# Optimization experiments

Hardware: AMD Instinct MI355X
Metric: run time of the kernel (lower is better)

## Reference

```python
import jax, jax.numpy as jnp
import numpy as np

N_NODES = 100000
N_EDGES = 1600000
HID = 128
EPS = 1e-5

def _bn(x, gamma, beta):
    # BatchNorm1d in training mode: biased batch stats over node dim
    mu = jnp.mean(x, axis=0)
    var = jnp.mean((x - mu) ** 2, axis=0)
    return (x - mu) * jax.lax.rsqrt(var + EPS) * gamma + beta

def _gcn(x, src, dst, norm, n, W, b):
    # PyG GCNConv: h = x @ W, symmetric-normalized aggregation with self-loops, + bias
    h = x @ W
    msg = h[src] * norm[:, None]            # [E+N, H] gather + scale
    out = jax.ops.segment_sum(msg, dst, num_segments=n)
    return out + b

def _gcn_norm(edge_index, n):
    # append self-loops, compute D^{-1/2}[src] * D^{-1/2}[dst]
    loop = jnp.arange(n, dtype=edge_index.dtype)
    src = jnp.concatenate([edge_index[0], loop])
    dst = jnp.concatenate([edge_index[1], loop])
    deg = jax.ops.segment_sum(jnp.ones_like(dst, dtype=jnp.float32), dst, num_segments=n)
    dinv = jax.lax.rsqrt(jnp.maximum(deg, 1.0))  # deg >= 1 due to self loops
    norm = dinv[src] * dinv[dst]
    return src, dst, norm

def setup_inputs() -> dict:
    key = jax.random.key(0)
    ks = jax.random.split(key, 20)
    def lin(k, fan_in, fan_out):
        bound = 1.0 / np.sqrt(fan_in)
        kw, kb = jax.random.split(k)
        W = jax.random.uniform(kw, (fan_in, fan_out), jnp.float32, -bound, bound)
        b = jax.random.uniform(kb, (fan_out,), jnp.float32, -bound, bound)
        return W, b
    x = jax.random.normal(ks[0], (N_NODES, 2), jnp.float32)
    edge_index = jax.random.randint(ks[1], (2, N_EDGES), 0, N_NODES, jnp.int32)
    We, be = lin(ks[2], 2, HID)
    W1, b1 = lin(ks[3], HID, HID)
    W2, b2 = lin(ks[4], HID, HID)
    W3, b3 = lin(ks[5], HID, HID)
    Wf1, bf1 = lin(ks[6], HID, 32)
    Wf2, bf2 = lin(ks[7], 32, 2)
    ones = lambda n: jnp.ones((n,), jnp.float32)
    zeros = lambda n: jnp.zeros((n,), jnp.float32)
    return dict(x=x, edge_index=edge_index, We=We, be=be,
                W1=W1, b1=b1, g1=ones(HID), bt1=zeros(HID),
                W2=W2, b2=b2, g2=ones(HID), bt2=zeros(HID),
                W3=W3, b3=b3, g3=ones(HID), bt3=zeros(HID),
                Wf1=Wf1, bf1=bf1, gf=ones(32), btf=zeros(32),
                Wf2=Wf2, bf2=bf2)

def reference(x, edge_index, We, be, W1, b1, g1, bt1, W2, b2, g2, bt2,
              W3, b3, g3, bt3, Wf1, bf1, gf, btf, Wf2, bf2):
    n = x.shape[0]
    src, dst, norm = _gcn_norm(edge_index, n)
    h = jax.nn.relu(x @ We + be)
    # block 1 with residual
    h1 = jax.nn.relu(_bn(_gcn(h, src, dst, norm, n, W1, b1), g1, bt1)) + h
    # block 2
    h2 = jax.nn.relu(_bn(_gcn(h1, src, dst, norm, n, W2, b2), g2, bt2)) + h1
    # block 3
    h3 = jax.nn.relu(_bn(_gcn(h2, src, dst, norm, n, W3, b3), g3, bt3)) + h2
    f = jax.nn.relu(_bn(h3 @ Wf1 + bf1, gf, btf))
    # dropout is identity in eval mode
    return jnp.tanh(f @ Wf2 + bf2)
```

## Files before the change

kernel.cpp:

```cpp
#include <hip/hip_runtime.h>
#include <hip/hip_fp16.h>
#include <math.h>

#define HID 128
#define EPS 1e-5f
#define BK 64
#define MAXNBK 2048
#define NSTRIPE 16
#define PADK 136

typedef _Float16 half8 __attribute__((ext_vector_type(8)));
typedef float f32x4 __attribute__((ext_vector_type(4)));


__global__ __launch_bounds__(256) void k_bhist(const int* __restrict__ dst, int* __restrict__ bcount,
                                               int e, int nbk) {
    __shared__ int hist[MAXNBK];
    for (int i = threadIdx.x; i < nbk; i += 256) hist[i] = 0;
    __syncthreads();
    int base = blockIdx.x * 4096;
    int end = min(base + 4096, e);
    for (int i = base + threadIdx.x; i < end; i += 256) atomicAdd(&hist[dst[i] >> 6], 1);
    __syncthreads();
    for (int i = threadIdx.x; i < nbk; i += 256) {
        int c = hist[i];
        if (c) atomicAdd(&bcount[i * 16], c);
    }
}

__global__ __launch_bounds__(1024) void k_bscan(const int* __restrict__ bcount, int* __restrict__ boffs,
                                                int* __restrict__ bcur, int nbk, int e) {
    __shared__ int lds[1024];
    int tid = threadIdx.x;
    int i0 = 2 * tid, i1 = 2 * tid + 1;
    int a = (i0 < nbk) ? bcount[i0 * 16] : 0;
    int b = (i1 < nbk) ? bcount[i1 * 16] : 0;
    lds[tid] = a + b;
    __syncthreads();
    for (int off = 1; off < 1024; off <<= 1) {
        int v = (tid >= off) ? lds[tid - off] : 0;
        __syncthreads();
        lds[tid] += v;
        __syncthreads();
    }
    int excl = lds[tid] - (a + b);
    if (i0 < nbk) { boffs[i0] = excl;     bcur[i0 * 16] = excl; }
    if (i1 < nbk) { boffs[i1] = excl + a; bcur[i1 * 16] = excl + a; }
    if (tid == 1023) boffs[nbk] = e;
}

__global__ __launch_bounds__(1024) void k_bscatter(const int* __restrict__ src, const int* __restrict__ dst,
                                                   int* __restrict__ bcur, int* __restrict__ btmp,
                                                   int e, int nbk) {
    __shared__ int hist[MAXNBK];
    int tid = threadIdx.x;
    for (int i = tid; i < nbk; i += 1024) hist[i] = 0;
    __syncthreads();
    int per = (e + gridDim.x - 1) / gridDim.x;
    int base = blockIdx.x * per;
    int end = min(base + per, e);
    for (int i = base + tid; i < end; i += 1024) atomicAdd(&hist[dst[i] >> 6], 1);
    __syncthreads();
    for (int i = tid; i < nbk; i += 1024) {
        int c = hist[i];
        hist[i] = c ? atomicAdd(&bcur[i * 16], c) : 0;
    }
    __syncthreads();
    for (int i = base + tid; i < end; i += 1024) {
        int d = dst[i];
        int pos = atomicAdd(&hist[d >> 6], 1);
        btmp[pos] = (src[i] << 6) | (d & 63);
    }
}

__global__ __launch_bounds__(256) void k_bsort(const int* __restrict__ btmp, const int* __restrict__ boffs,
                                               int* __restrict__ csr, int* __restrict__ offs,
                                               float* __restrict__ dinv, int n, int etot) {
    __shared__ int cnt[BK];
    __shared__ int cur[BK];
    int b = blockIdx.x, tid = threadIdx.x;
    if (tid < BK) cnt[tid] = 0;
    __syncthreads();
    int e0 = boffs[b], e1 = boffs[b + 1];
    for (int i = e0 + tid; i < e1; i += 256) atomicAdd(&cnt[btmp[i] & 63], 1);
    __syncthreads();
    if (tid == 0) {
        int run = 0;
        for (int d = 0; d < BK; ++d) { cur[d] = run; run += cnt[d]; }
    }
    __syncthreads();
    if (tid < BK) {
        int node = b * BK + tid;
        if (node < n) {
            offs[node] = e0 + cur[tid];
            dinv[node] = rsqrtf((float)(cnt[tid] + 1));
        }
    }
    if (b == 0 && tid == 0) offs[n] = etot;
    __syncthreads();
    for (int i = e0 + tid; i < e1; i += 256) {
        int p = btmp[i];
        int pos = e0 + atomicAdd(&cur[p & 63], 1);
        csr[pos] = p >> 6;
    }
}


__global__ void k_prepw(const float* __restrict__ W, _Float16* __restrict__ Wt) {
    int idx = blockIdx.x * 256 + threadIdx.x;
    int k = idx >> 7, nn = idx & 127;
    Wt[nn * 128 + k] = (_Float16)W[k * 128 + nn];
}

__global__ void k_prepwf(const float* __restrict__ W, _Float16* __restrict__ Wt) {
    int idx = blockIdx.x * 256 + threadIdx.x;
    int k = idx >> 5, nn = idx & 31;
    Wt[nn * 128 + k] = (_Float16)W[k * 32 + nn];
}


__global__ void k_embed(const float* __restrict__ x, const float* __restrict__ We,
                        const float* __restrict__ be, float* __restrict__ h, int n) {
    int i = blockIdx.x * 256 + threadIdx.x;
    if (i >= n * HID) return;
    int node = i >> 7, j = i & 127;
    float v = x[2 * node] * We[j] + x[2 * node + 1] * We[HID + j] + be[j];
    h[i] = fmaxf(v, 0.f);
}


__global__ __launch_bounds__(256) void k_mm1(const float* __restrict__ h, const _Float16* __restrict__ Wt,
                                             const float* __restrict__ dinv, __half2* __restrict__ th, int n) {
    __shared__ __attribute__((aligned(16))) _Float16 Ah[64][PADK];
    __shared__ __attribute__((aligned(16))) _Float16 Bh[128][PADK];
    int tid = threadIdx.x;
    int nb = blockIdx.x * 64;
    const float4* h4 = (const float4*)h;
#pragma unroll
    for (int r = 0; r < 8; ++r) {
        int idx = r * 256 + tid;
        int ni = idx >> 5, k4 = idx & 31;
        int node = nb + ni;
        float4 v = make_float4(0.f, 0.f, 0.f, 0.f);
        if (node < n) v = h4[(size_t)node * 32 + k4];
        union { __half2 h2[2]; uint2 u; } pk;
        pk.h2[0] = __floats2half2_rn(v.x, v.y);
        pk.h2[1] = __floats2half2_rn(v.z, v.w);
        *(uint2*)&Ah[ni][k4 * 4] = pk.u;
    }
    const uint4* wt4 = (const uint4*)Wt;
#pragma unroll
    for (int r = 0; r < 8; ++r) {
        int idx = r * 256 + tid;
        int row = idx >> 4, ch = idx & 15;
        *(uint4*)&Bh[row][ch * 8] = wt4[row * 16 + ch];
    }
    __syncthreads();
    int lane = tid & 63, w = tid >> 6;
    int mrow = lane & 15, quad = lane >> 4;
    f32x4 acc[8];
#pragma unroll
    for (int t = 0; t < 8; ++t) acc[t] = (f32x4){0.f, 0.f, 0.f, 0.f};
#pragma unroll
    for (int kc = 0; kc < 4; ++kc) {
        half8 av = *(half8*)&Ah[w * 16 + mrow][kc * 32 + quad * 8];
#pragma unroll
        for (int t = 0; t < 8; ++t) {
            half8 bv = *(half8*)&Bh[t * 16 + mrow][kc * 32 + quad * 8];
            acc[t] = __builtin_amdgcn_mfma_f32_16x16x32_f16(av, bv, acc[t], 0, 0, 0);
        }
    }
    float dv[4];
#pragma unroll
    for (int r = 0; r < 4; ++r) {
        int node = nb + w * 16 + quad * 4 + r;
        dv[r] = (node < n) ? dinv[node] : 0.f;
    }
    __syncthreads();
#pragma unroll
    for (int t = 0; t < 8; ++t)
#pragma unroll
        for (int r = 0; r < 4; ++r)
            Ah[w * 16 + quad * 4 + r][t * 16 + mrow] = (_Float16)(acc[t][r] * dv[r]);
    __syncthreads();
#pragma unroll
    for (int it = 0; it < 4; ++it) {
        int idx = it * 256 + tid;
        int row = idx >> 4, ch = idx & 15;
        int node = nb + row;
        if (node < n)
            ((uint4*)th)[(size_t)node * 16 + ch] = *(uint4*)&Ah[row][ch * 8];
    }
}


__global__ __launch_bounds__(256) void k_mmf(const float* __restrict__ agg, float* __restrict__ h,
                                             const float* __restrict__ A, const float* __restrict__ Cc,
                                             const _Float16* __restrict__ Wt, const float* __restrict__ dinv,
                                             __half2* __restrict__ th, int n) {
    __shared__ __attribute__((aligned(16))) _Float16 Ah[64][PADK];
    __shared__ __attribute__((aligned(16))) _Float16 Bh[128][PADK];
    __shared__ float As[128], Cs[128];
    int tid = threadIdx.x;
    int nb = blockIdx.x * 64;
    if (tid < 128) { As[tid] = A[tid]; Cs[tid] = Cc[tid]; }
    __syncthreads();
    const float4* a4p = (const float4*)agg;
    float4* h4 = (float4*)h;
#pragma unroll
    for (int r = 0; r < 8; ++r) {
        int idx = r * 256 + tid;
        int ni = idx >> 5, k4 = idx & 31;
        int node = nb + ni;
        float4 v = make_float4(0.f, 0.f, 0.f, 0.f);
        if (node < n) {
            float4 a = a4p[(size_t)node * 32 + k4];
            float4 ho = h4[(size_t)node * 32 + k4];
            float4 aa = *((const float4*)&As[k4 * 4]);
            float4 cc = *((const float4*)&Cs[k4 * 4]);
            v.x = fmaxf(a.x * aa.x + cc.x, 0.f) + ho.x;
            v.y = fmaxf(a.y * aa.y + cc.y, 0.f) + ho.y;
            v.z = fmaxf(a.z * aa.z + cc.z, 0.f) + ho.z;
            v.w = fmaxf(a.w * aa.w + cc.w, 0.f) + ho.w;
            h4[(size_t)node * 32 + k4] = v;
        }
        union { __half2 h2[2]; uint2 u; } pk;
        pk.h2[0] = __floats2half2_rn(v.x, v.y);
        pk.h2[1] = __floats2half2_rn(v.z, v.w);
        *(uint2*)&Ah[ni][k4 * 4] = pk.u;
    }
    const uint4* wt4 = (const uint4*)Wt;
#pragma unroll
    for (int r = 0; r < 8; ++r) {
        int idx = r * 256 + tid;
        int row = idx >> 4, ch = idx & 15;
        *(uint4*)&Bh[row][ch * 8] = wt4[row * 16 + ch];
    }
    __syncthreads();
    int lane = tid & 63, w = tid >> 6;
    int mrow = lane & 15, quad = lane >> 4;
    f32x4 acc[8];
#pragma unroll
    for (int t = 0; t < 8; ++t) acc[t] = (f32x4){0.f, 0.f, 0.f, 0.f};
#pragma unroll
    for (int kc = 0; kc < 4; ++kc) {
        half8 av = *(half8*)&Ah[w * 16 + mrow][kc * 32 + quad * 8];
#pragma unroll
        for (int t = 0; t < 8; ++t) {
            half8 bv = *(half8*)&Bh[t * 16 + mrow][kc * 32 + quad * 8];
            acc[t] = __builtin_amdgcn_mfma_f32_16x16x32_f16(av, bv, acc[t], 0, 0, 0);
        }
    }
    float dv[4];
#pragma unroll
    for (int r = 0; r < 4; ++r) {
        int node = nb + w * 16 + quad * 4 + r;
        dv[r] = (node < n) ? dinv[node] : 0.f;
    }
    __syncthreads();
#pragma unroll
    for (int t = 0; t < 8; ++t)
#pragma unroll
        for (int r = 0; r < 4; ++r)
            Ah[w * 16 + quad * 4 + r][t * 16 + mrow] = (_Float16)(acc[t][r] * dv[r]);
    __syncthreads();
#pragma unroll
    for (int it = 0; it < 4; ++it) {
        int idx = it * 256 + tid;
        int row = idx >> 4, ch = idx & 15;
        int node = nb + row;
        if (node < n)
            ((uint4*)th)[(size_t)node * 16 + ch] = *(uint4*)&Ah[row][ch * 8];
    }
}


__global__ __launch_bounds__(256) void k_mmh(const float* __restrict__ agg, const float* __restrict__ h,
                                             const float* __restrict__ A, const float* __restrict__ Cc,
                                             const _Float16* __restrict__ Wt, const float* __restrict__ bias,
                                             float* __restrict__ tf,
                                             float* __restrict__ S, float* __restrict__ SS, int n) {
    __shared__ __attribute__((aligned(16))) _Float16 Ah[64][PADK];
    __shared__ __attribute__((aligned(16))) _Float16 Bh[32][PADK];
    __shared__ float Ds[64][36];
    __shared__ float As[128], Cs[128];
    __shared__ float sredS[4][8][4], sredQ[4][8][4];
    int tid = threadIdx.x;
    int nb = blockIdx.x * 64;
    if (tid < 128) { As[tid] = A[tid]; Cs[tid] = Cc[tid]; }
    __syncthreads();
    const float4* a4p = (const float4*)agg;
    const float4* h4 = (const float4*)h;
#pragma unroll
    for (int r = 0; r < 8; ++r) {
        int idx = r * 256 + tid;
        int ni = idx >> 5, k4 = idx & 31;
        int node = nb + ni;
        float4 v = make_float4(0.f, 0.f, 0.f, 0.f);
        if (node < n) {
            float4 a = a4p[(size_t)node * 32 + k4];
            float4 ho = h4[(size_t)node * 32 + k4];
            float4 aa = *((const float4*)&As[k4 * 4]);
            float4 cc = *((const float4*)&Cs[k4 * 4]);
            v.x = fmaxf(a.x * aa.x + cc.x, 0.f) + ho.x;
            v.y = fmaxf(a.y * aa.y + cc.y, 0.f) + ho.y;
            v.z = fmaxf(a.z * aa.z + cc.z, 0.f) + ho.z;
            v.w = fmaxf(a.w * aa.w + cc.w, 0.f) + ho.w;
        }
        union { __half2 h2[2]; uint2 u; } pk;
        pk.h2[0] = __floats2half2_rn(v.x, v.y);
        pk.h2[1] = __floats2half2_rn(v.z, v.w);
        *(uint2*)&Ah[ni][k4 * 4] = pk.u;
    }
    const uint4* wt4 = (const uint4*)Wt;
#pragma unroll
    for (int r = 0; r < 2; ++r) {
        int idx = r * 256 + tid;
        int row = idx >> 4, ch = idx & 15;
        *(uint4*)&Bh[row][ch * 8] = wt4[row * 16 + ch];
    }
    __syncthreads();
    int lane = tid & 63, w = tid >> 6;
    int mrow = lane & 15, quad = lane >> 4;
    f32x4 acc[2];
    acc[0] = (f32x4){0.f, 0.f, 0.f, 0.f};
    acc[1] = (f32x4){0.f, 0.f, 0.f, 0.f};
#pragma unroll
    for (int kc = 0; kc < 4; ++kc) {
        half8 av = *(half8*)&Ah[w * 16 + mrow][kc * 32 + quad * 8];
#pragma unroll
        for (int t = 0; t < 2; ++t) {
            half8 bv = *(half8*)&Bh[t * 16 + mrow][kc * 32 + quad * 8];
            acc[t] = __builtin_amdgcn_mfma_f32_16x16x32_f16(av, bv, acc[t], 0, 0, 0);
        }
    }
#pragma unroll
    for (int t = 0; t < 2; ++t)
#pragma unroll
        for (int r = 0; r < 4; ++r)
            Ds[w * 16 + quad * 4 + r][t * 16 + mrow] = acc[t][r];
    __syncthreads();
    float ps0 = 0.f, ps1 = 0.f, ps2 = 0.f, ps3 = 0.f;
    float pq0 = 0.f, pq1 = 0.f, pq2 = 0.f, pq3 = 0.f;
    int c4 = tid & 7;
    float4 bb = ((const float4*)bias)[c4];
#pragma unroll
    for (int it = 0; it < 2; ++it) {
        int idx = it * 256 + tid;
        int row = idx >> 3;
        int node = nb + row;
        if (node < n) {
            float v0 = Ds[row][c4 * 4 + 0] + bb.x;
            float v1 = Ds[row][c4 * 4 + 1] + bb.y;
            float v2 = Ds[row][c4 * 4 + 2] + bb.z;
            float v3 = Ds[row][c4 * 4 + 3] + bb.w;
            *((float4*)&tf[(size_t)node * 32 + c4 * 4]) = make_float4(v0, v1, v2, v3);
            ps0 += v0; ps1 += v1; ps2 += v2; ps3 += v3;
            pq0 += v0 * v0; pq1 += v1 * v1; pq2 += v2 * v2; pq3 += v3 * v3;
        }
    }
#pragma unroll
    for (int off = 8; off < 64; off <<= 1) {
        ps0 += __shfl_down(ps0, off); ps1 += __shfl_down(ps1, off);
        ps2 += __shfl_down(ps2, off); ps3 += __shfl_down(ps3, off);
        pq0 += __shfl_down(pq0, off); pq1 += __shfl_down(pq1, off);
        pq2 += __shfl_down(pq2, off); pq3 += __shfl_down(pq3, off);
    }
    if (lane < 8) {
        sredS[w][lane][0] = ps0; sredS[w][lane][1] = ps1; sredS[w][lane][2] = ps2; sredS[w][lane][3] = ps3;
        sredQ[w][lane][0] = pq0; sredQ[w][lane][1] = pq1; sredQ[w][lane][2] = pq2; sredQ[w][lane][3] = pq3;
    }
    __syncthreads();
    if (tid < 32) {
        int cc4 = tid >> 2, j = tid & 3;
        float s = sredS[0][cc4][j] + sredS[1][cc4][j] + sredS[2][cc4][j] + sredS[3][cc4][j];
        float q = sredQ[0][cc4][j] + sredQ[1][cc4][j] + sredQ[2][cc4][j] + sredQ[3][cc4][j];
        int stripe = (blockIdx.x & (NSTRIPE - 1)) * 128;
        atomicAdd(&S[stripe + tid], s);
        atomicAdd(&SS[stripe + tid], q);
    }
}


__global__ __launch_bounds__(256) void k_agg(const __half2* __restrict__ t, const int* __restrict__ offs,
                                             const int* __restrict__ csr, const float* __restrict__ dinv,
                                             const float* __restrict__ bias, float* __restrict__ out,
                                             float* __restrict__ S, float* __restrict__ SS, int n) {
    __shared__ float ls[4][128];
    __shared__ float lss[4][128];
    int tid = threadIdx.x;
    int lane = tid & 63, w = tid >> 6;
    int sub = lane >> 5, fl = lane & 31;
    const uint2* t4 = (const uint2*)t;
    float4 bb = ((const float4*)bias)[fl];
    float s0 = 0.f, s1 = 0.f, s2 = 0.f, s3 = 0.f;
    float q0 = 0.f, q1 = 0.f, q2 = 0.f, q3 = 0.f;
    float selfm = (sub == 0) ? 1.f : 0.f;
    int ngrp = (n + 3) >> 2;
    for (int grp = blockIdx.x; grp < ngrp; grp += gridDim.x) {
        int node = grp * 4 + w;
        if (node < n) {
            uint2 rv = t4[(size_t)node * 32 + fl];
            float2 f0 = __half22float2(*(__half2*)&rv.x);
            float2 f1 = __half22float2(*(__half2*)&rv.y);
            float a0 = f0.x * selfm, a1 = f0.y * selfm, a2 = f1.x * selfm, a3 = f1.y * selfm;
            int e0 = offs[node], e1 = offs[node + 1];
            for (int e = e0; e < e1; e += 8) {
                int i0 = e + sub, i1 = e + 2 + sub, i2 = e + 4 + sub, i3 = e + 6 + sub;
                int c0 = csr[min(i0, e1 - 1)];
                int c1 = csr[min(i1, e1 - 1)];
                int c2 = csr[min(i2, e1 - 1)];
                int c3 = csr[min(i3, e1 - 1)];
                uint2 r0 = t4[(size_t)c0 * 32 + fl];
                uint2 r1 = t4[(size_t)c1 * 32 + fl];
                uint2 r2 = t4[(size_t)c2 * 32 + fl];
                uint2 r3 = t4[(size_t)c3 * 32 + fl];
                float m0 = (i0 < e1) ? 1.f : 0.f;
                float m1 = (i1 < e1) ? 1.f : 0.f;
                float m2 = (i2 < e1) ? 1.f : 0.f;
                float m3 = (i3 < e1) ? 1.f : 0.f;
                float2 g0 = __half22float2(*(__half2*)&r0.x), g1 = __half22float2(*(__half2*)&r0.y);
                a0 += m0 * g0.x; a1 += m0 * g0.y; a2 += m0 * g1.x; a3 += m0 * g1.y;
                g0 = __half22float2(*(__half2*)&r1.x); g1 = __half22float2(*(__half2*)&r1.y);
                a0 += m1 * g0.x; a1 += m1 * g0.y; a2 += m1 * g1.x; a3 += m1 * g1.y;
                g0 = __half22float2(*(__half2*)&r2.x); g1 = __half22float2(*(__half2*)&r2.y);
                a0 += m2 * g0.x; a1 += m2 * g0.y; a2 += m2 * g1.x; a3 += m2 * g1.y;
                g0 = __half22float2(*(__half2*)&r3.x); g1 = __half22float2(*(__half2*)&r3.y);
                a0 += m3 * g0.x; a1 += m3 * g0.y; a2 += m3 * g1.x; a3 += m3 * g1.y;
            }
            a0 += __shfl_down(a0, 32);
            a1 += __shfl_down(a1, 32);
            a2 += __shfl_down(a2, 32);
            a3 += __shfl_down(a3, 32);
            if (sub == 0) {
                float di = dinv[node];
                float v0 = a0 * di + bb.x, v1 = a1 * di + bb.y;
                float v2 = a2 * di + bb.z, v3 = a3 * di + bb.w;
                ((float4*)out)[(size_t)node * 32 + fl] = make_float4(v0, v1, v2, v3);
                s0 += v0; s1 += v1; s2 += v2; s3 += v3;
                q0 += v0 * v0; q1 += v1 * v1; q2 += v2 * v2; q3 += v3 * v3;
            }
        }
    }
    if (sub == 0) {
        ((float4*)&ls[w][0])[fl] = make_float4(s0, s1, s2, s3);
        ((float4*)&lss[w][0])[fl] = make_float4(q0, q1, q2, q3);
    }
    __syncthreads();
    if (tid < 128) {
        float s = ls[0][tid] + ls[1][tid] + ls[2][tid] + ls[3][tid];
        float q = lss[0][tid] + lss[1][tid] + lss[2][tid] + lss[3][tid];
        int stripe = (blockIdx.x & (NSTRIPE - 1)) * 128;
        atomicAdd(&S[stripe + tid], s);
        atomicAdd(&SS[stripe + tid], q);
    }
}


__global__ void k_bn_finalize(const float* __restrict__ S, const float* __restrict__ SS,
                              const float* __restrict__ g, const float* __restrict__ bt,
                              float* __restrict__ A, float* __restrict__ C, int n, int hid, int nstripe) {
    int j = threadIdx.x;
    if (j >= hid) return;
    float s = 0.f, q = 0.f;
    for (int k = 0; k < nstripe; ++k) { s += S[k * 128 + j]; q += SS[k * 128 + j]; }
    float mu = s / (float)n;
    float var = q / (float)n - mu * mu;
    float inv = rsqrtf(var + EPS);
    A[j] = g[j] * inv;
    C[j] = bt[j] - mu * g[j] * inv;
}


__global__ void k_final(const float* __restrict__ tf, const float* __restrict__ A,
                        const float* __restrict__ C, const float* __restrict__ Wf2,
                        const float* __restrict__ bf2, float* __restrict__ out, int n) {
    int node = blockIdx.x * 256 + threadIdx.x;
    if (node >= n) return;
    float o0 = bf2[0], o1 = bf2[1];
    const float4* t4 = (const float4*)(tf + (size_t)node * 32);
#pragma unroll
    for (int q = 0; q < 8; ++q) {
        float4 v = t4[q];
        float vv[4] = {v.x, v.y, v.z, v.w};
#pragma unroll
        for (int r = 0; r < 4; ++r) {
            int j = q * 4 + r;
            float f = fmaxf(vv[r] * A[j] + C[j], 0.f);
            o0 += f * Wf2[2 * j];
            o1 += f * Wf2[2 * j + 1];
        }
    }
    out[2 * node] = tanhf(o0);
    out[2 * node + 1] = tanhf(o1);
}


extern "C" void kernel_launch(void* const* d_in, const int* in_sizes, int n_in,
                              void* d_out, int out_size, void* d_ws, size_t ws_size,
                              hipStream_t stream) {
    const float* x   = (const float*)d_in[0];
    const int*   ei  = (const int*)d_in[1];
    const float* We  = (const float*)d_in[2];
    const float* be  = (const float*)d_in[3];
    const float* W1  = (const float*)d_in[4];
    const float* b1  = (const float*)d_in[5];
    const float* g1  = (const float*)d_in[6];
    const float* bt1 = (const float*)d_in[7];
    const float* W2  = (const float*)d_in[8];
    const float* b2  = (const float*)d_in[9];
    const float* g2  = (const float*)d_in[10];
    const float* bt2 = (const float*)d_in[11];
    const float* W3  = (const float*)d_in[12];
    const float* b3  = (const float*)d_in[13];
    const float* g3  = (const float*)d_in[14];
    const float* bt3 = (const float*)d_in[15];
    const float* Wf1 = (const float*)d_in[16];
    const float* bf1 = (const float*)d_in[17];
    const float* gf  = (const float*)d_in[18];
    const float* btf = (const float*)d_in[19];
    const float* Wf2 = (const float*)d_in[20];
    const float* bf2 = (const float*)d_in[21];
    float* out = (float*)d_out;

    const int n = in_sizes[0] / 2;
    const int e = in_sizes[1] / 2;
    const int* srcp = ei;
    const int* dstp = ei + e;
    const int nbk = (n + BK - 1) / BK;

    char* p = (char*)d_ws;
    auto alloc = [&](size_t bytes) { void* r = (void*)p; p += (bytes + 255) & ~(size_t)255; return r; };
    int*       bcount = (int*)alloc((size_t)nbk * 16 * 4);
    int*       boffs  = (int*)alloc((size_t)(nbk + 1) * 4);
    int*       bcur   = (int*)alloc((size_t)nbk * 16 * 4);
    int*       btmp   = (int*)alloc((size_t)e * 4);
    int*       csr    = (int*)alloc((size_t)e * 4);
    int*       offs   = (int*)alloc((size_t)(n + 1) * 4);
    float*     dinv   = (float*)alloc((size_t)n * 4);
    float*     h      = (float*)alloc((size_t)n * HID * 4);
    __half2*   th     = (__half2*)alloc((size_t)n * HID * 2);
    float*     agg    = (float*)alloc((size_t)n * HID * 4);
    float*     tf     = (float*)alloc((size_t)n * 32 * 4);
    float*     bnS    = (float*)alloc(NSTRIPE * 128 * 4);
    float*     bnSS   = (float*)alloc(NSTRIPE * 128 * 4);
    float*     bnA    = (float*)alloc(HID * 4);
    float*     bnC    = (float*)alloc(HID * 4);
    _Float16*  wt1    = (_Float16*)alloc(128 * 128 * 2);
    _Float16*  wt2    = (_Float16*)alloc(128 * 128 * 2);
    _Float16*  wt3    = (_Float16*)alloc(128 * 128 * 2);
    _Float16*  wtf    = (_Float16*)alloc(32 * 128 * 2);

    hipMemsetAsync(bcount, 0, (size_t)nbk * 16 * 4, stream);
    k_bhist<<<(e + 4095) / 4096, 256, 0, stream>>>(dstp, bcount, e, nbk);
    k_bscan<<<1, 1024, 0, stream>>>(bcount, boffs, bcur, nbk, e);
    k_bscatter<<<256, 1024, 0, stream>>>(srcp, dstp, bcur, btmp, e, nbk);
    k_bsort<<<nbk, 256, 0, stream>>>(btmp, boffs, csr, offs, dinv, n, e);
    k_prepw<<<64, 256, 0, stream>>>(W1, wt1);
    k_prepw<<<64, 256, 0, stream>>>(W2, wt2);
    k_prepw<<<64, 256, 0, stream>>>(W3, wt3);
    k_prepwf<<<16, 256, 0, stream>>>(Wf1, wtf);
    k_embed<<<(n * HID + 255) / 256, 256, 0, stream>>>(x, We, be, h, n);

    k_mm1<<<(n + 63) / 64, 256, 0, stream>>>(h, wt1, dinv, th, n);
    hipMemsetAsync(bnS, 0, NSTRIPE * 128 * 4, stream);
    hipMemsetAsync(bnSS, 0, NSTRIPE * 128 * 4, stream);
    k_agg<<<4096, 256, 0, stream>>>(th, offs, csr, dinv, b1, agg, bnS, bnSS, n);
    k_bn_finalize<<<1, 128, 0, stream>>>(bnS, bnSS, g1, bt1, bnA, bnC, n, 128, NSTRIPE);

    k_mmf<<<(n + 63) / 64, 256, 0, stream>>>(agg, h, bnA, bnC, wt2, dinv, th, n);
    hipMemsetAsync(bnS, 0, NSTRIPE * 128 * 4, stream);
    hipMemsetAsync(bnSS, 0, NSTRIPE * 128 * 4, stream);
    k_agg<<<4096, 256, 0, stream>>>(th, offs, csr, dinv, b2, agg, bnS, bnSS, n);
    k_bn_finalize<<<1, 128, 0, stream>>>(bnS, bnSS, g2, bt2, bnA, bnC, n, 128, NSTRIPE);

    k_mmf<<<(n + 63) / 64, 256, 0, stream>>>(agg, h, bnA, bnC, wt3, dinv, th, n);
    hipMemsetAsync(bnS, 0, NSTRIPE * 128 * 4, stream);
    hipMemsetAsync(bnSS, 0, NSTRIPE * 128 * 4, stream);
    k_agg<<<4096, 256, 0, stream>>>(th, offs, csr, dinv, b3, agg, bnS, bnSS, n);
    k_bn_finalize<<<1, 128, 0, stream>>>(bnS, bnSS, g3, bt3, bnA, bnC, n, 128, NSTRIPE);

    hipMemsetAsync(bnS, 0, NSTRIPE * 128 * 4, stream);
    hipMemsetAsync(bnSS, 0, NSTRIPE * 128 * 4, stream);
    k_mmh<<<(n + 63) / 64, 256, 0, stream>>>(agg, h, bnA, bnC, wtf, bf1, tf, bnS, bnSS, n);
    k_bn_finalize<<<1, 32, 0, stream>>>(bnS, bnSS, gf, btf, bnA, bnC, n, 32, NSTRIPE);
    k_final<<<(n + 255) / 256, 256, 0, stream>>>(tf, bnA, bnC, Wf2, bf2, out, n);
}
```

Baseline: 566.0 us.

## Fuse embed into first matmul, inline BN finalize, widen aggregation gathers

The embedding kernel is folded into k_mm1, which computes relu(x@We+be) on the fly, writes h and packs it to fp16 for the MFMA. This removes one full pass writing and re-reading h. The separate BN-finalize kernels and the per-layer memsets are removed: each consumer kernel reduces the stripe sums itself, and all stats buffers are cleared by one memset. The aggregation kernel now uses 16-byte gathers with 16 lanes per row and 4 edge sub-groups, which means more shuffle reduction and more registers per thread.

```diff
diff --git a/kernel.cpp b/kernel.cpp
--- a/kernel.cpp
+++ b/kernel.cpp
@@ -119,30 +119,36 @@
 }
 
 
-__global__ void k_embed(const float* __restrict__ x, const float* __restrict__ We,
-                        const float* __restrict__ be, float* __restrict__ h, int n) {
-    int i = blockIdx.x * 256 + threadIdx.x;
-    if (i >= n * HID) return;
-    int node = i >> 7, j = i & 127;
-    float v = x[2 * node] * We[j] + x[2 * node + 1] * We[HID + j] + be[j];
-    h[i] = fmaxf(v, 0.f);
-}
-
-
-__global__ __launch_bounds__(256) void k_mm1(const float* __restrict__ h, const _Float16* __restrict__ Wt,
-                                             const float* __restrict__ dinv, __half2* __restrict__ th, int n) {
+__global__ __launch_bounds__(256) void k_mm1(const float* __restrict__ x, const float* __restrict__ We,
+                                             const float* __restrict__ be, const _Float16* __restrict__ Wt,
+                                             const float* __restrict__ dinv, __half2* __restrict__ th,
+                                             float* __restrict__ h, int n) {
     __shared__ __attribute__((aligned(16))) _Float16 Ah[64][PADK];
     __shared__ __attribute__((aligned(16))) _Float16 Bh[128][PADK];
+    __shared__ float W0s[128], W1s[128], bes[128];
     int tid = threadIdx.x;
     int nb = blockIdx.x * 64;
-    const float4* h4 = (const float4*)h;
+    if (tid < 128) { W0s[tid] = We[tid]; W1s[tid] = We[128 + tid]; bes[tid] = be[tid]; }
+    __syncthreads();
+    float4* h4 = (float4*)h;
+    const float2* x2 = (const float2*)x;
 #pragma unroll
     for (int r = 0; r < 8; ++r) {
         int idx = r * 256 + tid;
         int ni = idx >> 5, k4 = idx & 31;
         int node = nb + ni;
         float4 v = make_float4(0.f, 0.f, 0.f, 0.f);
-        if (node < n) v = h4[(size_t)node * 32 + k4];
+        if (node < n) {
+            float2 xx = x2[node];
+            float4 w0 = *((const float4*)&W0s[k4 * 4]);
+            float4 w1 = *((const float4*)&W1s[k4 * 4]);
+            float4 bb = *((const float4*)&bes[k4 * 4]);
+            v.x = fmaxf(xx.x * w0.x + xx.y * w1.x + bb.x, 0.f);
+            v.y = fmaxf(xx.x * w0.y + xx.y * w1.y + bb.y, 0.f);
+            v.z = fmaxf(xx.x * w0.z + xx.y * w1.z + bb.z, 0.f);
+            v.w = fmaxf(xx.x * w0.w + xx.y * w1.w + bb.w, 0.f);
+            h4[(size_t)node * 32 + k4] = v;
+        }
         union { __half2 h2[2]; uint2 u; } pk;
         pk.h2[0] = __floats2half2_rn(v.x, v.y);
         pk.h2[1] = __floats2half2_rn(v.z, v.w);
@@ -195,7 +201,8 @@
 
 
 __global__ __launch_bounds__(256) void k_mmf(const float* __restrict__ agg, float* __restrict__ h,
-                                             const float* __restrict__ A, const float* __restrict__ Cc,
+                                             const float* __restrict__ S, const float* __restrict__ SS,
+                                             const float* __restrict__ g, const float* __restrict__ bt,
                                              const _Float16* __restrict__ Wt, const float* __restrict__ dinv,
                                              __half2* __restrict__ th, int n) {
     __shared__ __attribute__((aligned(16))) _Float16 Ah[64][PADK];
@@ -203,7 +210,16 @@
     __shared__ float As[128], Cs[128];
     int tid = threadIdx.x;
     int nb = blockIdx.x * 64;
-    if (tid < 128) { As[tid] = A[tid]; Cs[tid] = Cc[tid]; }
+    if (tid < 128) {
+        float s = 0.f, q = 0.f;
+#pragma unroll
+        for (int k = 0; k < NSTRIPE; ++k) { s += S[k * 128 + tid]; q += SS[k * 128 + tid]; }
+        float mu = s / (float)n;
+        float var = q / (float)n - mu * mu;
+        float inv = rsqrtf(var + EPS);
+        As[tid] = g[tid] * inv;
+        Cs[tid] = bt[tid] - mu * g[tid] * inv;
+    }
     __syncthreads();
     const float4* a4p = (const float4*)agg;
     float4* h4 = (float4*)h;
@@ -276,7 +292,8 @@
 
 
 __global__ __launch_bounds__(256) void k_mmh(const float* __restrict__ agg, const float* __restrict__ h,
-                                             const float* __restrict__ A, const float* __restrict__ Cc,
+                                             const float* __restrict__ Sin, const float* __restrict__ SSin,
+                                             const float* __restrict__ g, const float* __restrict__ bt,
                                              const _Float16* __restrict__ Wt, const float* __restrict__ bias,
                                              float* __restrict__ tf,
                                              float* __restrict__ S, float* __restrict__ SS, int n) {
@@ -287,7 +304,16 @@
     __shared__ float sredS[4][8][4], sredQ[4][8][4];
     int tid = threadIdx.x;
     int nb = blockIdx.x * 64;
-    if (tid < 128) { As[tid] = A[tid]; Cs[tid] = Cc[tid]; }
+    if (tid < 128) {
+        float s = 0.f, q = 0.f;
+#pragma unroll
+        for (int k = 0; k < NSTRIPE; ++k) { s += Sin[k * 128 + tid]; q += SSin[k * 128 + tid]; }
+        float mu = s / (float)n;
+        float var = q / (float)n - mu * mu;
+        float inv = rsqrtf(var + EPS);
+        As[tid] = g[tid] * inv;
+        Cs[tid] = bt[tid] - mu * g[tid] * inv;
+    }
     __syncthreads();
     const float4* a4p = (const float4*)agg;
     const float4* h4 = (const float4*)h;
@@ -390,61 +416,85 @@
     __shared__ float lss[4][128];
     int tid = threadIdx.x;
     int lane = tid & 63, w = tid >> 6;
-    int sub = lane >> 5, fl = lane & 31;
-    const uint2* t4 = (const uint2*)t;
-    float4 bb = ((const float4*)bias)[fl];
-    float s0 = 0.f, s1 = 0.f, s2 = 0.f, s3 = 0.f;
-    float q0 = 0.f, q1 = 0.f, q2 = 0.f, q3 = 0.f;
+    int sub = lane >> 4, fl = lane & 15;
+    const uint4* t8 = (const uint4*)t;
+    float4 bb0 = ((const float4*)bias)[fl * 2];
+    float4 bb1 = ((const float4*)bias)[fl * 2 + 1];
+    float st[8] = {0.f, 0.f, 0.f, 0.f, 0.f, 0.f, 0.f, 0.f};
+    float qt[8] = {0.f, 0.f, 0.f, 0.f, 0.f, 0.f, 0.f, 0.f};
     float selfm = (sub == 0) ? 1.f : 0.f;
     int ngrp = (n + 3) >> 2;
     for (int grp = blockIdx.x; grp < ngrp; grp += gridDim.x) {
         int node = grp * 4 + w;
         if (node < n) {
-            uint2 rv = t4[(size_t)node * 32 + fl];
-            float2 f0 = __half22float2(*(__half2*)&rv.x);
-            float2 f1 = __half22float2(*(__half2*)&rv.y);
-            float a0 = f0.x * selfm, a1 = f0.y * selfm, a2 = f1.x * selfm, a3 = f1.y * selfm;
+            float a[8];
+            {
+                uint4 rv = t8[(size_t)node * 16 + fl];
+                float2 f0 = __half22float2(*(__half2*)&rv.x);
+                float2 f1 = __half22float2(*(__half2*)&rv.y);
+                float2 f2 = __half22float2(*(__half2*)&rv.z);
+                float2 f3 = __half22float2(*(__half2*)&rv.w);
+                a[0] = f0.x * selfm; a[1] = f0.y * selfm; a[2] = f1.x * selfm; a[3] = f1.y * selfm;
+                a[4] = f2.x * selfm; a[5] = f2.y * selfm; a[6] = f3.x * selfm; a[7] = f3.y * selfm;
+            }
             int e0 = offs[node], e1 = offs[node + 1];
-            for (int e = e0; e < e1; e += 8) {
-                int i0 = e + sub, i1 = e + 2 + sub, i2 = e + 4 + sub, i3 = e + 6 + sub;
+            for (int e = e0; e < e1; e += 16) {
+                int i0 = e + sub, i1 = e + 4 + sub, i2 = e + 8 + sub, i3 = e + 12 + sub;
                 int c0 = csr[min(i0, e1 - 1)];
                 int c1 = csr[min(i1, e1 - 1)];
                 int c2 = csr[min(i2, e1 - 1)];
                 int c3 = csr[min(i3, e1 - 1)];
-                uint2 r0 = t4[(size_t)c0 * 32 + fl];
-                uint2 r1 = t4[(size_t)c1 * 32 + fl];
-                uint2 r2 = t4[(size_t)c2 * 32 + fl];
-                uint2 r3 = t4[(size_t)c3 * 32 + fl];
+                uint4 r0 = t8[(size_t)c0 * 16 + fl];
+                uint4 r1 = t8[(size_t)c1 * 16 + fl];
+                uint4 r2 = t8[(size_t)c2 * 16 + fl];
+                uint4 r3 = t8[(size_t)c3 * 16 + fl];
                 float m0 = (i0 < e1) ? 1.f : 0.f;
                 float m1 = (i1 < e1) ? 1.f : 0.f;
                 float m2 = (i2 < e1) ? 1.f : 0.f;
                 float m3 = (i3 < e1) ? 1.f : 0.f;
-                float2 g0 = __half22float2(*(__half2*)&r0.x), g1 = __half22float2(*(__half2*)&r0.y);
-                a0 += m0 * g0.x; a1 += m0 * g0.y; a2 += m0 * g1.x; a3 += m0 * g1.y;
+                float2 g0, g1, g2, g3;
+                g0 = __half22float2(*(__half2*)&r0.x); g1 = __half22float2(*(__half2*)&r0.y);
+                g2 = __half22float2(*(__half2*)&r0.z); g3 = __half22float2(*(__half2*)&r0.w);
+                a[0] += m0 * g0.x; a[1] += m0 * g0.y; a[2] += m0 * g1.x; a[3] += m0 * g1.y;
+                a[4] += m0 * g2.x; a[5] += m0 * g2.y; a[6] += m0 * g3.x; a[7] += m0 * g3.y;
                 g0 = __half22float2(*(__half2*)&r1.x); g1 = __half22float2(*(__half2*)&r1.y);
-                a0 += m1 * g0.x; a1 += m1 * g0.y; a2 += m1 * g1.x; a3 += m1 * g1.y;
+                g2 = __half22float2(*(__half2*)&r1.z); g3 = __half22float2(*(__half2*)&r1.w);
+                a[0] += m1 * g0.x; a[1] += m1 * g0.y; a[2] += m1 * g1.x; a[3] += m1 * g1.y;
+                a[4] += m1 * g2.x; a[5] += m1 * g2.y; a[6] += m1 * g3.x; a[7] += m1 * g3.y;
                 g0 = __half22float2(*(__half2*)&r2.x); g1 = __half22float2(*(__half2*)&r2.y);
-                a0 += m2 * g0.x; a1 += m2 * g0.y; a2 += m2 * g1.x; a3 += m2 * g1.y;
+                g2 = __half22float2(*(__half2*)&r2.z); g3 = __half22float2(*(__half2*)&r2.w);
+                a[0] += m2 * g0.x; a[1] += m2 * g0.y; a[2] += m2 * g1.x; a[3] += m2 * g1.y;
+                a[4] += m2 * g2.x; a[5] += m2 * g2.y; a[6] += m2 * g3.x; a[7] += m2 * g3.y;
                 g0 = __half22float2(*(__half2*)&r3.x); g1 = __half22float2(*(__half2*)&r3.y);
-                a0 += m3 * g0.x; a1 += m3 * g0.y; a2 += m3 * g1.x; a3 += m3 * g1.y;
+                g2 = __half22float2(*(__half2*)&r3.z); g3 = __half22float2(*(__half2*)&r3.w);
+                a[0] += m3 * g0.x; a[1] += m3 * g0.y; a[2] += m3 * g1.x; a[3] += m3 * g1.y;
+                a[4] += m3 * g2.x; a[5] += m3 * g2.y; a[6] += m3 * g3.x; a[7] += m3 * g3.y;
             }
-            a0 += __shfl_down(a0, 32);
-            a1 += __shfl_down(a1, 32);
-            a2 += __shfl_down(a2, 32);
-            a3 += __shfl_down(a3, 32);
+#pragma unroll
+            for (int j = 0; j < 8; ++j) {
+                a[j] += __shfl_down(a[j], 16);
+                a[j] += __shfl_down(a[j], 32);
+            }
             if (sub == 0) {
                 float di = dinv[node];
-                float v0 = a0 * di + bb.x, v1 = a1 * di + bb.y;
-                float v2 = a2 * di + bb.z, v3 = a3 * di + bb.w;
-                ((float4*)out)[(size_t)node * 32 + fl] = make_float4(v0, v1, v2, v3);
-                s0 += v0; s1 += v1; s2 += v2; s3 += v3;
-                q0 += v0 * v0; q1 += v1 * v1; q2 += v2 * v2; q3 += v3 * v3;
+                float v0 = a[0] * di + bb0.x, v1 = a[1] * di + bb0.y;
+                float v2 = a[2] * di + bb0.z, v3 = a[3] * di + bb0.w;
+                float v4 = a[4] * di + bb1.x, v5 = a[5] * di + bb1.y;
+                float v6 = a[6] * di + bb1.z, v7 = a[7] * di + bb1.w;
+                ((float4*)out)[(size_t)node * 32 + fl * 2] = make_float4(v0, v1, v2, v3);
+                ((float4*)out)[(size_t)node * 32 + fl * 2 + 1] = make_float4(v4, v5, v6, v7);
+                st[0] += v0; st[1] += v1; st[2] += v2; st[3] += v3;
+                st[4] += v4; st[5] += v5; st[6] += v6; st[7] += v7;
+                qt[0] += v0 * v0; qt[1] += v1 * v1; qt[2] += v2 * v2; qt[3] += v3 * v3;
+                qt[4] += v4 * v4; qt[5] += v5 * v5; qt[6] += v6 * v6; qt[7] += v7 * v7;
             }
         }
     }
     if (sub == 0) {
-        ((float4*)&ls[w][0])[fl] = make_float4(s0, s1, s2, s3);
-        ((float4*)&lss[w][0])[fl] = make_float4(q0, q1, q2, q3);
+        *(float4*)&ls[w][fl * 8] = make_float4(st[0], st[1], st[2], st[3]);
+        *(float4*)&ls[w][fl * 8 + 4] = make_float4(st[4], st[5], st[6], st[7]);
+        *(float4*)&lss[w][fl * 8] = make_float4(qt[0], qt[1], qt[2], qt[3]);
+        *(float4*)&lss[w][fl * 8 + 4] = make_float4(qt[4], qt[5], qt[6], qt[7]);
     }
     __syncthreads();
     if (tid < 128) {
@@ -457,25 +507,25 @@
 }
 
 
-__global__ void k_bn_finalize(const float* __restrict__ S, const float* __restrict__ SS,
-                              const float* __restrict__ g, const float* __restrict__ bt,
-                              float* __restrict__ A, float* __restrict__ C, int n, int hid, int nstripe) {
-    int j = threadIdx.x;
-    if (j >= hid) return;
-    float s = 0.f, q = 0.f;
-    for (int k = 0; k < nstripe; ++k) { s += S[k * 128 + j]; q += SS[k * 128 + j]; }
-    float mu = s / (float)n;
-    float var = q / (float)n - mu * mu;
-    float inv = rsqrtf(var + EPS);
-    A[j] = g[j] * inv;
-    C[j] = bt[j] - mu * g[j] * inv;
-}
-
-
-__global__ void k_final(const float* __restrict__ tf, const float* __restrict__ A,
-                        const float* __restrict__ C, const float* __restrict__ Wf2,
-                        const float* __restrict__ bf2, float* __restrict__ out, int n) {
-    int node = blockIdx.x * 256 + threadIdx.x;
+__global__ __launch_bounds__(256) void k_final(const float* __restrict__ tf,
+                                               const float* __restrict__ S, const float* __restrict__ SS,
+                                               const float* __restrict__ gf, const float* __restrict__ btf,
+                                               const float* __restrict__ Wf2, const float* __restrict__ bf2,
+                                               float* __restrict__ out, int n) {
+    __shared__ float Af[32], Cf[32];
+    int tid = threadIdx.x;
+    if (tid < 32) {
+        float s = 0.f, q = 0.f;
+#pragma unroll
+        for (int k = 0; k < NSTRIPE; ++k) { s += S[k * 128 + tid]; q += SS[k * 128 + tid]; }
+        float mu = s / (float)n;
+        float var = q / (float)n - mu * mu;
+        float inv = rsqrtf(var + EPS);
+        Af[tid] = gf[tid] * inv;
+        Cf[tid] = btf[tid] - mu * gf[tid] * inv;
+    }
+    __syncthreads();
+    int node = blockIdx.x * 256 + tid;
     if (node >= n) return;
     float o0 = bf2[0], o1 = bf2[1];
     const float4* t4 = (const float4*)(tf + (size_t)node * 32);
@@ -486,7 +536,7 @@
 #pragma unroll
         for (int r = 0; r < 4; ++r) {
             int j = q * 4 + r;
-            float f = fmaxf(vv[r] * A[j] + C[j], 0.f);
+            float f = fmaxf(vv[r] * Af[j] + Cf[j], 0.f);
             o0 += f * Wf2[2 * j];
             o1 += f * Wf2[2 * j + 1];
         }
@@ -542,16 +592,19 @@
     __half2*   th     = (__half2*)alloc((size_t)n * HID * 2);
     float*     agg    = (float*)alloc((size_t)n * HID * 4);
     float*     tf     = (float*)alloc((size_t)n * 32 * 4);
-    float*     bnS    = (float*)alloc(NSTRIPE * 128 * 4);
-    float*     bnSS   = (float*)alloc(NSTRIPE * 128 * 4);
-    float*     bnA    = (float*)alloc(HID * 4);
-    float*     bnC    = (float*)alloc(HID * 4);
+    float*     bnAll  = (float*)alloc(8 * NSTRIPE * 128 * 4);
     _Float16*  wt1    = (_Float16*)alloc(128 * 128 * 2);
     _Float16*  wt2    = (_Float16*)alloc(128 * 128 * 2);
     _Float16*  wt3    = (_Float16*)alloc(128 * 128 * 2);
     _Float16*  wtf    = (_Float16*)alloc(32 * 128 * 2);
 
+    float* S0 = bnAll;             float* SS0 = bnAll + 4 * NSTRIPE * 128;
+    float* S1 = S0 + NSTRIPE*128;  float* SS1 = SS0 + NSTRIPE*128;
+    float* S2 = S1 + NSTRIPE*128;  float* SS2 = SS1 + NSTRIPE*128;
+    float* SH = S2 + NSTRIPE*128;  float* SSH = SS2 + NSTRIPE*128;
+
     hipMemsetAsync(bcount, 0, (size_t)nbk * 16 * 4, stream);
+    hipMemsetAsync(bnAll, 0, 8 * NSTRIPE * 128 * 4, stream);
     k_bhist<<<(e + 4095) / 4096, 256, 0, stream>>>(dstp, bcount, e, nbk);
     k_bscan<<<1, 1024, 0, stream>>>(bcount, boffs, bcur, nbk, e);
     k_bscatter<<<256, 1024, 0, stream>>>(srcp, dstp, bcur, btmp, e, nbk);
@@ -560,29 +613,17 @@
     k_prepw<<<64, 256, 0, stream>>>(W2, wt2);
     k_prepw<<<64, 256, 0, stream>>>(W3, wt3);
     k_prepwf<<<16, 256, 0, stream>>>(Wf1, wtf);
-    k_embed<<<(n * HID + 255) / 256, 256, 0, stream>>>(x, We, be, h, n);
-
-    k_mm1<<<(n + 63) / 64, 256, 0, stream>>>(h, wt1, dinv, th, n);
-    hipMemsetAsync(bnS, 0, NSTRIPE * 128 * 4, stream);
-    hipMemsetAsync(bnSS, 0, NSTRIPE * 128 * 4, stream);
-    k_agg<<<4096, 256, 0, stream>>>(th, offs, csr, dinv, b1, agg, bnS, bnSS, n);
-    k_bn_finalize<<<1, 128, 0, stream>>>(bnS, bnSS, g1, bt1, bnA, bnC, n, 128, NSTRIPE);
-
-    k_mmf<<<(n + 63) / 64, 256, 0, stream>>>(agg, h, bnA, bnC, wt2, dinv, th, n);
-    hipMemsetAsync(bnS, 0, NSTRIPE * 128 * 4, stream);
-    hipMemsetAsync(bnSS, 0, NSTRIPE * 128 * 4, stream);
-    k_agg<<<4096, 256, 0, stream>>>(th, offs, csr, dinv, b2, agg, bnS, bnSS, n);
-    k_bn_finalize<<<1, 128, 0, stream>>>(bnS, bnSS, g2, bt2, bnA, bnC, n, 128, NSTRIPE);
-
-    k_mmf<<<(n + 63) / 64, 256, 0, stream>>>(agg, h, bnA, bnC, wt3, dinv, th, n);
-    hipMemsetAsync(bnS, 0, NSTRIPE * 128 * 4, stream);
-    hipMemsetAsync(bnSS, 0, NSTRIPE * 128 * 4, stream);
-    k_agg<<<4096, 256, 0, stream>>>(th, offs, csr, dinv, b3, agg, bnS, bnSS, n);
-    k_bn_finalize<<<1, 128, 0, stream>>>(bnS, bnSS, g3, bt3, bnA, bnC, n, 128, NSTRIPE);
-
-    hipMemsetAsync(bnS, 0, NSTRIPE * 128 * 4, stream);
-    hipMemsetAsync(bnSS, 0, NSTRIPE * 128 * 4, stream);
-    k_mmh<<<(n + 63) / 64, 256, 0, stream>>>(agg, h, bnA, bnC, wtf, bf1, tf, bnS, bnSS, n);
-    k_bn_finalize<<<1, 32, 0, stream>>>(bnS, bnSS, gf, btf, bnA, bnC, n, 32, NSTRIPE);
-    k_final<<<(n + 255) / 256, 256, 0, stream>>>(tf, bnA, bnC, Wf2, bf2, out, n);
-}
+
+    k_mm1<<<(n + 63) / 64, 256, 0, stream>>>(x, We, be, wt1, dinv, th, h, n);
+    k_agg<<<4096, 256, 0, stream>>>(th, offs, csr, dinv, b1, agg, S0, SS0, n);
+
+    k_mmf<<<(n + 63) / 64, 256, 0, stream>>>(agg, h, S0, SS0, g1, bt1, wt2, dinv, th, n);
+    k_agg<<<4096, 256, 0, stream>>>(th, offs, csr, dinv, b2, agg, S1, SS1, n);
+
+    k_mmf<<<(n + 63) / 64, 256, 0, stream>>>(agg, h, S1, SS1, g2, bt2, wt3, dinv, th, n);
+    k_agg<<<4096, 256, 0, stream>>>(th, offs, csr, dinv, b3, agg, S2, SS2, n);
+
+    k_mmh<<<(n + 63) / 64, 256, 0, stream>>>(agg, h, S2, SS2, g3, bt3, wtf, bf1, tf, SH, SSH, n);
+
+    k_final<<<(n + 255) / 256, 256, 0, stream>>>(tf, SH, SSH, gf, btf, Wf2, bf2, out, n);
+}
```

Result: faster. 533.3 us (-5.8%).
